# Performance work log

Measured on AMD Instinct MI355X. Metric: run time of the kernel, lower is better.

Reference implementation:

```python
import jax, jax.numpy as jnp
import numpy as np


def setup_inputs() -> dict:
    key = jax.random.key(0)
    kx, ky, kw = jax.random.split(key, 3)
    B, N, M = 8, 4096, 4096
    x = jax.random.normal(kx, (B, N, 3), dtype=jnp.float32)
    y = jax.random.normal(ky, (B, M, 3), dtype=jnp.float32)
    weight = jax.random.uniform(kw, (B,), dtype=jnp.float32)
    return {"x": x, "y": y, "weight": weight}


def reference(x, y, weight):
    # (mathematically identical to sum((x-y)^2), avoids the (B,N,M,3) tensor)
    x2 = jnp.sum(x * x, axis=-1)                     # (B, N)
    y2 = jnp.sum(y * y, axis=-1)                     # (B, M)
    xy = jnp.einsum('bnd,bmd->bnm', x, y)            # (B, N, M)
    dist = jnp.maximum(x2[:, :, None] + y2[:, None, :] - 2.0 * xy, 0.0)
    dist_x_min = jnp.min(dist, axis=2)               # (B, N) nearest-in-y per x
    dist_y_min = jnp.min(dist, axis=1)               # (B, M) nearest-in-x per y
    # point_reduction='mean', bidirectional=True
    loss = jnp.mean(dist_x_min, axis=1) + jnp.mean(dist_y_min, axis=1)  # (B,)
    loss = loss * weight
    # batch_reduction='mean'
    return jnp.mean(loss)
```

## Files before the change

kernel.cpp:

```cpp
#include <hip/hip_runtime.h>
#include <math.h>


constexpr int BATCH = 8;
constexpr int NP    = 4096;
constexpr int MC    = 16;
constexpr int MCH   = 256;
constexpr int KPT   = 8;
constexpr int T     = 256;

constexpr size_t PMIN_STRIDE = (size_t)BATCH * MC * NP;
constexpr size_t PS_OFF      = 2 * PMIN_STRIDE;

__global__ __launch_bounds__(T) void chamfer_partial(
    const float* __restrict__ x, const float* __restrict__ y,
    float* __restrict__ ws)
{
    const int bid = blockIdx.x;
    const int dir = bid >> 8;
    const int r   = bid & 255;
    const int b   = r >> 5;
    const int xc  = (r >> 4) & 1;
    const int mc  = r & 15;

    const float* q = dir ? y : x;
    const float* t = dir ? x : y;

    __shared__ float4 ty[MCH];
    const int tid = threadIdx.x;

    const float* tb = t + (size_t)(b * NP + mc * MCH) * 3;
    {
        float t0 = tb[3 * tid + 0];
        float t1 = tb[3 * tid + 1];
        float t2 = tb[3 * tid + 2];
        ty[tid] = make_float4(t0, t1, t2, fmaf(t0, t0, fmaf(t1, t1, t2 * t2)));
    }

    const int n0 = b * NP + xc * 2048 + tid * KPT;
    const float4* qb = reinterpret_cast<const float4*>(q + (size_t)n0 * 3);
    float4 v0 = qb[0], v1 = qb[1], v2 = qb[2], v3 = qb[3], v4 = qb[4], v5 = qb[5];
    float px[KPT][3] = {
        {v0.x, v0.y, v0.z}, {v0.w, v1.x, v1.y},
        {v1.z, v1.w, v2.x}, {v2.y, v2.z, v2.w},
        {v3.x, v3.y, v3.z}, {v3.w, v4.x, v4.y},
        {v4.z, v4.w, v5.x}, {v5.y, v5.z, v5.w},
    };
    float xn[KPT][3], x2s[KPT], mn[KPT];
    #pragma unroll
    for (int k = 0; k < KPT; ++k) {
        x2s[k] = fmaf(px[k][0], px[k][0], fmaf(px[k][1], px[k][1], px[k][2] * px[k][2]));
        #pragma unroll
        for (int d = 0; d < 3; ++d) xn[k][d] = -2.0f * px[k][d];
        mn[k] = INFINITY;
    }

    __syncthreads();

    #pragma unroll 4
    for (int j = 0; j < MCH; ++j) {
        float4 tv = ty[j];
        #pragma unroll
        for (int k = 0; k < KPT; ++k) {
            float d = fmaf(xn[k][2], tv.z, tv.w);
            d = fmaf(xn[k][1], tv.y, d);
            d = fmaf(xn[k][0], tv.x, d);
            mn[k] = fminf(mn[k], d);
        }
    }

    float4 o0, o1;
    o0.x = fmaxf(x2s[0] + mn[0], 0.0f);
    o0.y = fmaxf(x2s[1] + mn[1], 0.0f);
    o0.z = fmaxf(x2s[2] + mn[2], 0.0f);
    o0.w = fmaxf(x2s[3] + mn[3], 0.0f);
    o1.x = fmaxf(x2s[4] + mn[4], 0.0f);
    o1.y = fmaxf(x2s[5] + mn[5], 0.0f);
    o1.z = fmaxf(x2s[6] + mn[6], 0.0f);
    o1.w = fmaxf(x2s[7] + mn[7], 0.0f);

    float* pm = ws + (size_t)dir * PMIN_STRIDE
                   + ((size_t)(b * MC + mc)) * NP
                   + (size_t)xc * 2048 + (size_t)tid * KPT;
    reinterpret_cast<float4*>(pm)[0] = o0;
    reinterpret_cast<float4*>(pm)[1] = o1;
}

__global__ __launch_bounds__(T) void chamfer_combine(
    const float* __restrict__ ws, float* __restrict__ ps)
{
    const int bid = blockIdx.x;
    const int dir = bid >> 5;
    const int b   = (bid >> 2) & 7;
    const int nq  = bid & 3;
    const int tid = threadIdx.x;

    const float* base = ws + (size_t)dir * PMIN_STRIDE + (size_t)b * MC * NP;

    float sum = 0.0f;
    #pragma unroll
    for (int i = 0; i < 4; ++i) {
        const int n = nq * 1024 + i * 256 + tid;
        float v = INFINITY;
        #pragma unroll
        for (int m = 0; m < MC; ++m) v = fminf(v, base[(size_t)m * NP + n]);
        sum += v;
    }

    for (int off = 32; off; off >>= 1) sum += __shfl_down(sum, off, 64);
    __shared__ float red[4];
    if ((tid & 63) == 0) red[tid >> 6] = sum;
    __syncthreads();
    if (tid == 0) ps[bid] = (red[0] + red[1]) + (red[2] + red[3]);
}

__global__ void chamfer_final(
    const float* __restrict__ ps, const float* __restrict__ w,
    float* __restrict__ out)
{
    const int l = threadIdx.x;
    float v = ps[l];
    const int b = (l >> 2) & 7;
    float acc = v * w[b] * (1.0f / ((float)NP * (float)BATCH));
    for (int off = 32; off; off >>= 1) acc += __shfl_down(acc, off, 64);
    if (l == 0) out[0] = acc;
}

extern "C" void kernel_launch(void* const* d_in, const int* in_sizes, int n_in,
                              void* d_out, int out_size, void* d_ws, size_t ws_size,
                              hipStream_t stream) {
    const float* x = (const float*)d_in[0];
    const float* y = (const float*)d_in[1];
    const float* w = (const float*)d_in[2];
    float* out = (float*)d_out;
    float* ws  = (float*)d_ws;

    chamfer_partial<<<512, T, 0, stream>>>(x, y, ws);
    chamfer_combine<<<64, T, 0, stream>>>(ws, ws + PS_OFF);
    chamfer_final<<<1, 64, 0, stream>>>(ws + PS_OFF, w, out);
}
```

Measured before the change: 30.42 us.

## Fuse final reduction into combine via atomic counter and use v_min3 in inner loop

Removes the third kernel launch: the combine kernel now uses 256 blocks, each block writes a weighted partial sum, and the last block to finish (found through an atomic counter reset in the partial kernel) does the final reduction. The inner distance loop processes two target points per iteration and merges them with a single v_min3_f32 instruction, cutting min operations. It also spreads the combine work over more blocks. The cost is extra atomics and fences, plus the counter reset depending on launch ordering.

Measured after the change: 35.59 us. +17.0%, slower.

```diff
diff --git a/kernel.cpp b/kernel.cpp
--- a/kernel.cpp
+++ b/kernel.cpp
@@ -11,12 +11,17 @@
 
 constexpr size_t PMIN_STRIDE = (size_t)BATCH * MC * NP;
 constexpr size_t PS_OFF      = 2 * PMIN_STRIDE;
+constexpr int    PS_N        = 256;
+constexpr size_t CTR_OFF     = PS_OFF + PS_N;
 
 __global__ __launch_bounds__(T) void chamfer_partial(
     const float* __restrict__ x, const float* __restrict__ y,
     float* __restrict__ ws)
 {
     const int bid = blockIdx.x;
+    if (bid == 0 && threadIdx.x == 0) {
+        *reinterpret_cast<unsigned int*>(ws + CTR_OFF) = 0u;
+    }
     const int dir = bid >> 8;
     const int r   = bid & 255;
     const int b   = r >> 5;
@@ -58,14 +63,21 @@
     __syncthreads();
 
     #pragma unroll 4
-    for (int j = 0; j < MCH; ++j) {
-        float4 tv = ty[j];
+    for (int j = 0; j < MCH; j += 2) {
+        float4 ta = ty[j];
+        float4 tc = ty[j + 1];
         #pragma unroll
         for (int k = 0; k < KPT; ++k) {
-            float d = fmaf(xn[k][2], tv.z, tv.w);
-            d = fmaf(xn[k][1], tv.y, d);
-            d = fmaf(xn[k][0], tv.x, d);
-            mn[k] = fminf(mn[k], d);
+            float da = fmaf(xn[k][2], ta.z, ta.w);
+            da = fmaf(xn[k][1], ta.y, da);
+            da = fmaf(xn[k][0], ta.x, da);
+            float db = fmaf(xn[k][2], tc.z, tc.w);
+            db = fmaf(xn[k][1], tc.y, db);
+            db = fmaf(xn[k][0], tc.x, db);
+            float m;
+            asm("v_min3_f32 %0, %1, %2, %3"
+                : "=v"(m) : "v"(mn[k]), "v"(da), "v"(db));
+            mn[k] = m;
         }
     }
 
@@ -87,43 +99,52 @@
 }
 
 __global__ __launch_bounds__(T) void chamfer_combine(
-    const float* __restrict__ ws, float* __restrict__ ps)
+    float* __restrict__ ws, const float* __restrict__ w,
+    float* __restrict__ out)
 {
     const int bid = blockIdx.x;
-    const int dir = bid >> 5;
-    const int b   = (bid >> 2) & 7;
-    const int nq  = bid & 3;
+    const int dir = bid >> 7;
+    const int b   = (bid >> 4) & 7;
+    const int nq  = bid & 15;
     const int tid = threadIdx.x;
 
     const float* base = ws + (size_t)dir * PMIN_STRIDE + (size_t)b * MC * NP;
+    float* ps = ws + PS_OFF;
+    unsigned int* ctr = reinterpret_cast<unsigned int*>(ws + CTR_OFF);
 
-    float sum = 0.0f;
+    const int n = nq * 256 + tid;
+    float v = INFINITY;
     #pragma unroll
-    for (int i = 0; i < 4; ++i) {
-        const int n = nq * 1024 + i * 256 + tid;
-        float v = INFINITY;
-        #pragma unroll
-        for (int m = 0; m < MC; ++m) v = fminf(v, base[(size_t)m * NP + n]);
-        sum += v;
-    }
+    for (int m = 0; m < MC; ++m) v = fminf(v, base[(size_t)m * NP + n]);
 
+    float sum = v;
     for (int off = 32; off; off >>= 1) sum += __shfl_down(sum, off, 64);
     __shared__ float red[4];
+    __shared__ int lastflag;
     if ((tid & 63) == 0) red[tid >> 6] = sum;
     __syncthreads();
-    if (tid == 0) ps[bid] = (red[0] + red[1]) + (red[2] + red[3]);
-}
 
-__global__ void chamfer_final(
-    const float* __restrict__ ps, const float* __restrict__ w,
-    float* __restrict__ out)
-{
-    const int l = threadIdx.x;
-    float v = ps[l];
-    const int b = (l >> 2) & 7;
-    float acc = v * w[b] * (1.0f / ((float)NP * (float)BATCH));
-    for (int off = 32; off; off >>= 1) acc += __shfl_down(acc, off, 64);
-    if (l == 0) out[0] = acc;
+    if (tid == 0) {
+        float bs = (red[0] + red[1]) + (red[2] + red[3]);
+        bs *= w[b] * (1.0f / ((float)NP * (float)BATCH));
+        __hip_atomic_store(&ps[bid], bs, __ATOMIC_RELEASE,
+                           __HIP_MEMORY_SCOPE_AGENT);
+        __threadfence();
+        unsigned int old = atomicAdd(ctr, 1u);
+        lastflag = (old == 255u) ? 1 : 0;
+    }
+    __syncthreads();
+
+    if (lastflag) {
+        __threadfence();
+        float p = __hip_atomic_load(&ps[tid], __ATOMIC_ACQUIRE,
+                                    __HIP_MEMORY_SCOPE_AGENT);
+        float acc = p;
+        for (int off = 32; off; off >>= 1) acc += __shfl_down(acc, off, 64);
+        if ((tid & 63) == 0) red[tid >> 6] = acc;
+        __syncthreads();
+        if (tid == 0) out[0] = (red[0] + red[1]) + (red[2] + red[3]);
+    }
 }
 
 extern "C" void kernel_launch(void* const* d_in, const int* in_sizes, int n_in,
@@ -136,6 +157,5 @@
     float* ws  = (float*)d_ws;
 
     chamfer_partial<<<512, T, 0, stream>>>(x, y, ws);
-    chamfer_combine<<<64, T, 0, stream>>>(ws, ws + PS_OFF);
-    chamfer_final<<<1, 64, 0, stream>>>(ws + PS_OFF, w, out);
+    chamfer_combine<<<256, T, 0, stream>>>(ws, w, out);
 }
```
